# Performance work log

Measured on AMD Instinct MI355X. Metric: run time of the kernel, lower is better.

Reference implementation:

```python
import jax, jax.numpy as jnp
import numpy as np

SQ2PI = 0.79788456
M, D_IN, H1, H2, D_OUT = 256, 784, 256, 256, 10


def setup_inputs() -> dict:
    key = jax.random.key(0)
    ks = jax.random.split(key, 6)
    x = jax.random.normal(ks[0], (M, D_IN), dtype=jnp.float32)
    target = jax.random.randint(ks[1], (M,), 0, D_OUT)

    def init_w(k, fan_in, fan_out):
        # torch init: uniform(-1/sqrt(size(1)), 1/sqrt(size(1))) * scale (scale=1)
        stdv = 1.0 / np.sqrt(fan_out)
        return jax.random.uniform(k, (fan_in, fan_out), jnp.float32, -stdv, stdv)

    w0 = init_w(ks[2], D_IN, H1)
    w1 = init_w(ks[3], H1, H2)
    w2 = init_w(ks[4], H2, H2)
    wlast = init_w(ks[5], H2, D_OUT)
    th0 = jnp.zeros((1, H1), jnp.float32)
    th1 = jnp.zeros((1, H2), jnp.float32)
    th2 = jnp.zeros((1, H2), jnp.float32)
    thlast = jnp.zeros((1, D_OUT), jnp.float32)
    return dict(x=x, target=target, w0=w0, w1=w1, w2=w2, wlast=wlast,
                th0=th0, th1=th1, th2=th2, thlast=thlast)


def _mvg_layer(xbar, xcov, m, th):
    # sigma[b] = m^T @ xcov[b] @ m + diag(sum_j 1 - m[j,:]^2)
    s = jnp.sum(1.0 - m ** 2, axis=0)                      # [H2]
    t = jnp.einsum('bjk,kl->bjl', xcov, m)                 # [B,H,H2]
    sigma = jnp.einsum('ji,bjl->bil', m, t) + jnp.diag(s)[None]  # [B,H2,H2]
    diagsig = jnp.diagonal(sigma, axis1=1, axis2=2)        # [B,H2]
    hbar = xbar @ m + th                                   # [B,H2]
    xbar_next = jnp.tanh(SQ2PI * hbar / jnp.sqrt(diagsig))
    c = (1.0 - xbar_next ** 2) / jnp.sqrt(diagsig)         # [B,H2]
    eye = jnp.eye(m.shape[1], dtype=xbar.dtype)
    xcov_next = (SQ2PI * sigma * c[:, :, None] * c[:, None, :]
                 + eye[None] * (1.0 - xbar_next[:, None, :] ** 2))
    return xbar_next, xcov_next


def reference(x, target, w0, w1, w2, wlast, th0, th1, th2, thlast):
    m0 = 2.0 * jax.nn.sigmoid(w0) - 1.0
    m1 = 2.0 * jax.nn.sigmoid(w1) - 1.0
    m2 = 2.0 * jax.nn.sigmoid(w2) - 1.0
    mlast = 2.0 * jax.nn.sigmoid(wlast) - 1.0

    # first layer: xcov for input is implicitly zero, sigma is diagonal
    diagsig1 = jnp.sum(1.0 - m0 ** 2, axis=0)              # [H1]
    h1bar = x @ m0 + th0                                   # [M,H1]
    x1bar = jnp.tanh(SQ2PI * h1bar / jnp.sqrt(diagsig1))
    eye1 = jnp.eye(m0.shape[1], dtype=x.dtype)
    xcov1 = eye1[None] * (1.0 - x1bar[:, None, :] ** 2)    # [M,H1,H1]

    x2bar, xcov2 = _mvg_layer(x1bar, xcov1, m1, th1)
    x3bar, xcov3 = _mvg_layer(x2bar, xcov2, m2, th2)

    hlastbar = x3bar @ mlast + thlast                      # [M,10]
    logprobs = jax.nn.log_softmax(hlastbar, axis=-1)
    loss = -jnp.mean(jnp.take_along_axis(logprobs, target[:, None], axis=1))
    pred = jnp.argmax(hlastbar, axis=1)
    frac_correct = jnp.mean((pred == target).astype(jnp.float32))
    return (hlastbar, logprobs, xcov3, loss, frac_correct)
```

## Files before the change

kernel.cpp:

```cpp
#include <hip/hip_runtime.h>
#include <hip/hip_fp8.h>
#include <math.h>

#define SQ2PI_F 0.79788456f

typedef __attribute__((ext_vector_type(8))) short short8;
typedef __attribute__((ext_vector_type(4))) float f32x4;
typedef __attribute__((ext_vector_type(4))) unsigned short u16x4;
typedef __attribute__((address_space(1))) unsigned int gas_u32;
typedef __attribute__((address_space(3))) unsigned int las_u32;

__device__ inline unsigned short bf16rne(float x) {
  unsigned int u = __float_as_uint(x);
  u += 0x7fffu + ((u >> 16) & 1u);
  return (unsigned short)(u >> 16);
}
__device__ inline float bf2f(unsigned short u) {
  return __uint_as_float(((unsigned int)u) << 16);
}
__device__ inline unsigned int pk_fp8x4(f32x4 v) {
  __hip_fp8_e4m3 a(v[0]), b(v[1]), c(v[2]), d(v[3]);
  return (unsigned int)a.__x | ((unsigned int)b.__x << 8) |
         ((unsigned int)c.__x << 16) | ((unsigned int)d.__x << 24);
}
__device__ inline float fp8tof(unsigned char b) {
  __hip_fp8_e4m3 h;
  h.__x = (__hip_fp8_storage_t)b;
  return (float)h;
}

__global__ void k_prep(const float* __restrict__ w0, const float* __restrict__ w1,
                       const float* __restrict__ w2, const float* __restrict__ wlast,
                       float* __restrict__ m0, float* __restrict__ m1,
                       unsigned short* __restrict__ m1th, float* __restrict__ m2,
                       unsigned short* __restrict__ m2th, unsigned char* __restrict__ m2f8,
                       float* __restrict__ mlast, float* __restrict__ lf) {
  int b = blockIdx.x, t = threadIdx.x;
  if (b < 784) {
    int i = b * 256 + t;
    m0[i] = tanhf(0.5f * w0[i]);
  } else if (b < 1040) {
    int j = b - 784;
    float v = tanhf(0.5f * w1[j * 256 + t]);
    m1[j * 256 + t] = v;
    m1th[t * 256 + j] = bf16rne(v);
  } else if (b < 1296) {
    int j = b - 1040;
    float v = tanhf(0.5f * w2[j * 256 + t]);
    m2[j * 256 + t] = v;
    m2th[t * 256 + j] = bf16rne(v);
    m2f8[t * 256 + j] = __hip_fp8_e4m3(v).__x;
  } else {
    int i = (b - 1296) * 256 + t;
    if (i < 2560) mlast[i] = tanhf(0.5f * wlast[i]);
    if (b == 1296 && t < 2) lf[t] = 0.f;
  }
}

__global__ void k_layer1(const float* __restrict__ x, const float* __restrict__ m0,
                         const float* __restrict__ th0,
                         float* __restrict__ x1bar, float* __restrict__ d1) {
  __shared__ float xr[784];
  __shared__ float ph[256], pd[256];
  int r = blockIdx.x, t = threadIdx.x;
  int j = t & 255, h = t >> 8;
  for (int p = t; p < 784; p += 512) xr[p] = x[r * 784 + p];
  __syncthreads();
  float acch = 0.f, accd = 0.f;
  int k0 = h * 392, k1 = k0 + 392;
#pragma unroll 8
  for (int k = k0; k < k1; ++k) {
    float mm = m0[k * 256 + j];
    acch = fmaf(xr[k], mm, acch);
    accd = fmaf(-mm, mm, accd + 1.f);
  }
  if (h) { ph[j] = acch; pd[j] = accd; }
  __syncthreads();
  if (!h) {
    acch += ph[j];
    accd += pd[j];
    float rs = rsqrtf(accd);
    float xb = tanhf(SQ2PI_F * (acch + th0[j]) * rs);
    x1bar[r * 256 + j] = xb;
    d1[r * 256 + j] = 1.f - xb * xb;
  }
}

__global__ void k_layer2(const float* __restrict__ d1, const float* __restrict__ x1bar,
                         const float* __restrict__ m1, const float* __restrict__ m2,
                         const float* __restrict__ th1, const float* __restrict__ th2,
                         float* __restrict__ c2, float* __restrict__ d2p,
                         float* __restrict__ h3bar,
                         float* __restrict__ s1g, float* __restrict__ s2g) {
  __shared__ float pd[256], ph[256], ps[256], sx[256], p3[256], q2[256];
  int r = blockIdx.x, t = threadIdx.x;
  int i = t & 255, h = t >> 8;
  int j0 = h * 128, j1 = j0 + 128;
  float accd = 0.f, acch = 0.f, accs = 0.f;
  for (int j = j0; j < j1; ++j) {
    float mm = m1[j * 256 + i];
    accd = fmaf(d1[r * 256 + j] * mm, mm, accd);
    acch = fmaf(x1bar[r * 256 + j], mm, acch);
    accs = fmaf(-mm, mm, accs + 1.f);
  }
  if (h) { pd[i] = accd; ph[i] = acch; ps[i] = accs; }
  __syncthreads();
  if (!h) {
    accd += pd[i];
    acch += ph[i];
    accs += ps[i];
    float rs = rsqrtf(accd + accs);
    float xb = tanhf(SQ2PI_F * (acch + th1[i]) * rs);
    float d = 1.f - xb * xb;
    c2[r * 256 + i] = d * rs;
    d2p[r * 256 + i] = d;
    sx[i] = xb;
    if (r == 0) s1g[i] = accs;
  }
  __syncthreads();
  float acc3 = 0.f, acc2 = 0.f;
  for (int j = j0; j < j1; ++j) {
    float mm = m2[j * 256 + i];
    acc3 = fmaf(sx[j], mm, acc3);
    acc2 = fmaf(-mm, mm, acc2 + 1.f);
  }
  if (h) { p3[i] = acc3; q2[i] = acc2; }
  __syncthreads();
  if (!h) {
    h3bar[r * 256 + i] = acc3 + p3[i] + th2[i];
    if (r == 0) s2g[i] = acc2 + q2[i];
  }
}

__global__ __launch_bounds__(1024) void k_fused(
    const unsigned short* __restrict__ m1th, const unsigned short* __restrict__ m2th,
    const unsigned char* __restrict__ m2f8, const float* __restrict__ d1,
    const float* __restrict__ c2, const float* __restrict__ d2p,
    const float* __restrict__ s1, const float* __restrict__ s2,
    const float* __restrict__ h3bar, float* __restrict__ x3bar,
    float* __restrict__ xcov3) {
  __shared__ __align__(16) unsigned char XC[65536];
  __shared__ __align__(16) unsigned short SB[2][8192];
  __shared__ float c2L[256], d2pL[256], s1L[256], s2L[256];
  __shared__ float c3L[256], d3L[256];
  __shared__ float pq[1024];

  const int b = blockIdx.x;
  const int tid = threadIdx.x;
  const int l = tid & 63, w = tid >> 6;
  const int lr = l & 15, lk = l >> 4;
  const int R = w * 16;

  auto stage_panel = [&](const unsigned short* gsrc, unsigned short* sb) {
    int rl = w * 2 + (l >> 5);
    int ch = l & 31;
    const unsigned short* src = gsrc + rl * 256 + ((ch ^ (rl & 7)) << 3);
    unsigned short* dst = sb + (w * 2) * 256;
    __builtin_amdgcn_global_load_lds((const gas_u32*)src, (las_u32*)dst, 16, 0, 0);
  };

#define PREAD(SBASE, p, kc)                                   \
  (*(const short8*)((const char*)(SBASE) + ((p) << 9) +      \
                    ((unsigned)((((kc) ^ ((p) & 7))) << 4))))

  stage_panel(m1th, SB[0]);

  if (tid < 256) {
    c2L[tid] = c2[b * 256 + tid];
    d2pL[tid] = d2p[b * 256 + tid];
    s1L[tid] = s1[tid];
    s2L[tid] = s2[tid];
  }

  const float* d1b = d1 + b * 256;

  short8 af_w[8];
#pragma unroll
  for (int ks = 0; ks < 8; ++ks) {
    f32x4 dv0 = *(const f32x4*)(d1b + ks * 32 + lk * 8);
    f32x4 dv1 = *(const f32x4*)(d1b + ks * 32 + lk * 8 + 4);
    short8 mv = *(const short8*)(m1th + (size_t)(R + lr) * 256 + ks * 32 + lk * 8);
#pragma unroll
    for (int e = 0; e < 4; ++e) {
      af_w[ks][e] = (short)bf16rne(bf2f((unsigned short)mv[e]) * dv0[e]);
      af_w[ks][e + 4] = (short)bf16rne(bf2f((unsigned short)mv[e + 4]) * dv1[e]);
    }
  }
  __syncthreads();

  short8 afX[8];
  unsigned short(*XB)[8192] = (unsigned short(*)[8192])XC;

#pragma unroll
  for (int cp = 0; cp < 8; ++cp) {
    if (cp < 7)
      stage_panel(m1th + (size_t)(cp + 1) * 8192, SB[(cp + 1) & 1]);
    else
      stage_panel(m2th, SB[0]);
    const unsigned short* sbc = SB[cp & 1];
    f32x4 acc[2];
    acc[0] = {0.f, 0.f, 0.f, 0.f};
    acc[1] = {0.f, 0.f, 0.f, 0.f};
#pragma unroll
    for (int ks = 0; ks < 8; ++ks) {
      short8 bq0 = PREAD(sbc, lr, ks * 4 + lk);
      short8 bq1 = PREAD(sbc, 16 + lr, ks * 4 + lk);
      acc[0] = __builtin_amdgcn_mfma_f32_16x16x32_bf16(af_w[ks], bq0, acc[0], 0, 0, 0);
      acc[1] = __builtin_amdgcn_mfma_f32_16x16x32_bf16(af_w[ks], bq1, acc[1], 0, 0, 0);
    }
    char* XP = (char*)XB[cp & 1];
    int r0 = R + lk * 4;
#pragma unroll
    for (int j = 0; j < 2; ++j) {
      int p = j * 16 + lr;
      int cc = cp * 32 + p;
      float c2c = c2L[cc];
      u16x4 st;
#pragma unroll
      for (int e = 0; e < 4; ++e) {
        int r = r0 + e;
        float g = acc[j][e];
        if (r == cc) g += s1L[r];
        float v = SQ2PI_F * c2L[r] * c2c * g;
        if (r == cc) v += d2pL[r];
        st[e] = bf16rne(v);
      }
      *(u16x4*)(XP + (p << 9) + (((unsigned)(r0 << 1)) ^ ((p & 7) << 4))) = st;
    }
    __syncthreads();
    if (cp == (w >> 1)) {
      int p2 = (w & 1) * 16 + lr;
#pragma unroll
      for (int ks = 0; ks < 8; ++ks) afX[ks] = PREAD(XP, p2, ks * 4 + lk);
    }
  }

#pragma unroll
  for (int lp = 0; lp < 8; ++lp) {
    if (lp < 7) stage_panel(m2th + (size_t)(lp + 1) * 8192, SB[(lp + 1) & 1]);
    const unsigned short* sbt = SB[lp & 1];
    f32x4 at[2];
    at[0] = {0.f, 0.f, 0.f, 0.f};
    at[1] = {0.f, 0.f, 0.f, 0.f};
#pragma unroll
    for (int ks = 0; ks < 8; ++ks) {
      short8 bq0 = PREAD(sbt, lr, ks * 4 + lk);
      short8 bq1 = PREAD(sbt, 16 + lr, ks * 4 + lk);
      at[0] = __builtin_amdgcn_mfma_f32_16x16x32_bf16(afX[ks], bq0, at[0], 0, 0, 0);
      at[1] = __builtin_amdgcn_mfma_f32_16x16x32_bf16(afX[ks], bq1, at[1], 0, 0, 0);
    }
    int j0 = R + lk * 4;
#pragma unroll
    for (int jf = 0; jf < 2; ++jf) {
      int lq = lp * 32 + jf * 16 + lr;
      unsigned int pk = pk_fp8x4(at[jf]);
      *(unsigned int*)(XC + (lq << 8) + ((((j0 >> 3) ^ (lq & 7)) << 3) + (j0 & 7))) = pk;
    }
    __syncthreads();
  }

  {
    int lq = tid >> 2, q = tid & 3;
    float s = 0.f;
#pragma unroll
    for (int jc = q * 8; jc < q * 8 + 8; ++jc) {
      unsigned long long c8 =
          *(const unsigned long long*)(XC + (lq << 8) + ((jc ^ (lq & 7)) << 3));
      short8 mv = *(const short8*)(m2th + (size_t)lq * 256 + jc * 8);
#pragma unroll
      for (int e = 0; e < 8; ++e)
        s = fmaf(bf2f((unsigned short)mv[e]), fp8tof((unsigned char)(c8 >> (8 * e))), s);
    }
    pq[tid] = s;
  }
  __syncthreads();

  if (tid < 256) {
    float ds = pq[tid * 4] + pq[tid * 4 + 1] + pq[tid * 4 + 2] + pq[tid * 4 + 3] + s2L[tid];
    float rs = rsqrtf(ds);
    float xb = tanhf(SQ2PI_F * h3bar[b * 256 + tid] * rs);
    x3bar[b * 256 + tid] = xb;
    float d = 1.f - xb * xb;
    c3L[tid] = d * rs;
    d3L[tid] = d;
  }
  __syncthreads();

  long am2[8];
#pragma unroll
  for (int ks = 0; ks < 8; ++ks)
    am2[ks] = *(const long*)(m2f8 + (size_t)(R + lr) * 256 + ks * 32 + lk * 8);

#pragma unroll
  for (int lp = 0; lp < 8; ++lp) {
    f32x4 sc[2];
    sc[0] = {0.f, 0.f, 0.f, 0.f};
    sc[1] = {0.f, 0.f, 0.f, 0.f};
    int p0 = lp * 32 + lr, p1 = lp * 32 + 16 + lr;
#pragma unroll
    for (int ks = 0; ks < 8; ++ks) {
      long bq0 = *(const long*)(XC + (p0 << 8) + (((ks * 4 + lk) ^ (p0 & 7)) << 3));
      long bq1 = *(const long*)(XC + (p1 << 8) + (((ks * 4 + lk) ^ (p1 & 7)) << 3));
      sc[0] = __builtin_amdgcn_mfma_f32_16x16x32_fp8_fp8(am2[ks], bq0, sc[0], 0, 0, 0);
      sc[1] = __builtin_amdgcn_mfma_f32_16x16x32_fp8_fp8(am2[ks], bq1, sc[1], 0, 0, 0);
    }
    int i0 = R + lk * 4;
#pragma unroll
    for (int lf = 0; lf < 2; ++lf) {
      int gl = lp * 32 + lf * 16 + lr;
      float cg = c3L[gl];
      f32x4 st;
#pragma unroll
      for (int e = 0; e < 4; ++e) {
        int i = i0 + e;
        float g = sc[lf][e];
        if (i == gl) g += s2L[i];
        float v = SQ2PI_F * c3L[i] * cg * g;
        if (i == gl) v += d3L[i];
        st[e] = v;
      }
      *(f32x4*)(xcov3 + ((size_t)b << 16) + (size_t)gl * 256 + i0) = st;
    }
  }
#undef PREAD
}

__global__ void k_final4(const float* __restrict__ x3bar, const float* __restrict__ mlast,
                         const float* __restrict__ thlast, const int* __restrict__ target,
                         float* __restrict__ hlast_out, float* __restrict__ logp_out,
                         float* __restrict__ loss_out, float* __restrict__ frac_out) {
  __shared__ float Wl[2560];
  int t = threadIdx.x;
  int r = blockIdx.x * 64 + t;
  for (int p = t; p < 2560; p += 64) Wl[p] = mlast[p];
  __syncthreads();
  float acc[10];
#pragma unroll
  for (int c = 0; c < 10; ++c) acc[c] = thlast[c];
  for (int j = 0; j < 256; ++j) {
    float xv = x3bar[r * 256 + j];
#pragma unroll
    for (int c = 0; c < 10; ++c) acc[c] = fmaf(xv, Wl[j * 10 + c], acc[c]);
  }
#pragma unroll
  for (int c = 0; c < 10; ++c) hlast_out[r * 10 + c] = acc[c];
  float mx = acc[0];
  int am = 0;
#pragma unroll
  for (int c = 1; c < 10; ++c)
    if (acc[c] > mx) { mx = acc[c]; am = c; }
  float se = 0.f;
#pragma unroll
  for (int c = 0; c < 10; ++c) se += expf(acc[c] - mx);
  float lse = logf(se);
#pragma unroll
  for (int c = 0; c < 10; ++c) logp_out[r * 10 + c] = acc[c] - mx - lse;
  int tg = target[r];
  float lossc = -(acc[tg] - mx - lse) * (1.f / 256.f);
  float corr = (am == tg) ? (1.f / 256.f) : 0.f;
#pragma unroll
  for (int off = 32; off > 0; off >>= 1) {
    lossc += __shfl_down(lossc, off);
    corr += __shfl_down(corr, off);
  }
  if (t == 0) {
    atomicAdd(loss_out, lossc);
    atomicAdd(frac_out, corr);
  }
}


extern "C" void kernel_launch(void* const* d_in, const int* in_sizes, int n_in,
                              void* d_out, int out_size, void* d_ws, size_t ws_size,
                              hipStream_t stream) {
  const float* x = (const float*)d_in[0];
  const int* target = (const int*)d_in[1];
  const float* w0 = (const float*)d_in[2];
  const float* w1 = (const float*)d_in[3];
  const float* w2 = (const float*)d_in[4];
  const float* wlast = (const float*)d_in[5];
  const float* th0 = (const float*)d_in[6];
  const float* th1 = (const float*)d_in[7];
  const float* th2 = (const float*)d_in[8];
  const float* thlast = (const float*)d_in[9];

  float* W = (float*)d_ws;
  size_t o = 0;
  auto alloc = [&](size_t n) { float* p = W + o; o += n; return p; };
  float* m0 = alloc(200704);
  float* m1 = alloc(65536);
  float* m2 = alloc(65536);
  float* mlast = alloc(2560);
  float* s1 = alloc(256);
  float* s2 = alloc(256);
  float* x1bar = alloc(65536);
  float* d1 = alloc(65536);
  float* c2 = alloc(65536);
  float* d2p = alloc(65536);
  float* h3bar = alloc(65536);
  float* x3bar = alloc(65536);
  unsigned short* m1th = (unsigned short*)alloc(32768);
  unsigned short* m2th = (unsigned short*)alloc(32768);
  unsigned char* m2f8 = (unsigned char*)alloc(16384);

  float* hlast = (float*)d_out;
  float* logp = hlast + 2560;
  float* xcov3_out = logp + 2560;
  float* loss = xcov3_out + 16777216;
  float* frac = loss + 1;

  k_prep<<<1306, 256, 0, stream>>>(w0, w1, w2, wlast, m0, m1, m1th, m2, m2th,
                                   m2f8, mlast, loss);
  k_layer1<<<256, 512, 0, stream>>>(x, m0, th0, x1bar, d1);
  k_layer2<<<256, 512, 0, stream>>>(d1, x1bar, m1, m2, th1, th2, c2, d2p,
                                    h3bar, s1, s2);
  k_fused<<<256, 1024, 0, stream>>>(m1th, m2th, m2f8, d1, c2, d2p, s1, s2,
                                    h3bar, x3bar, xcov3_out);
  k_final4<<<4, 64, 0, stream>>>(x3bar, mlast, thlast, target, hlast, logp, loss, frac);
}
```

Measured before the change: 138.8 us.

## Widen panels to 64 columns, fuse diagonal-sigma reduction, pad fp8 tile layout

Doubles the staged weight panel width from 32 to 64 rows, so each wave issues four MFMAs per k-step and the kernel takes half as many panel iterations and barriers. The separate pass that computed the diagonal of sigma from the fp8 tile and global m2 is removed. That sum is now built inside the second GEMM loop from fp32 accumulators and the LDS-staged m2 panel, using shuffles and LDS atomics. The fp8 tile moves from an XOR swizzle to a 264-byte padded row stride, and __launch_bounds__ gains a second argument of 4. LDS use roughly doubles for the staging buffers, and the atomics and wider accumulators raise register and LDS pressure.

```diff
diff --git a/kernel.cpp b/kernel.cpp
--- a/kernel.cpp
+++ b/kernel.cpp
@@ -22,11 +22,6 @@
   __hip_fp8_e4m3 a(v[0]), b(v[1]), c(v[2]), d(v[3]);
   return (unsigned int)a.__x | ((unsigned int)b.__x << 8) |
          ((unsigned int)c.__x << 16) | ((unsigned int)d.__x << 24);
-}
-__device__ inline float fp8tof(unsigned char b) {
-  __hip_fp8_e4m3 h;
-  h.__x = (__hip_fp8_storage_t)b;
-  return (float)h;
 }
 
 __global__ void k_prep(const float* __restrict__ w0, const float* __restrict__ w1,
@@ -132,18 +127,17 @@
   }
 }
 
-__global__ __launch_bounds__(1024) void k_fused(
+__global__ __launch_bounds__(1024, 4) void k_fused(
     const unsigned short* __restrict__ m1th, const unsigned short* __restrict__ m2th,
     const unsigned char* __restrict__ m2f8, const float* __restrict__ d1,
     const float* __restrict__ c2, const float* __restrict__ d2p,
     const float* __restrict__ s1, const float* __restrict__ s2,
     const float* __restrict__ h3bar, float* __restrict__ x3bar,
     float* __restrict__ xcov3) {
-  __shared__ __align__(16) unsigned char XC[65536];
-  __shared__ __align__(16) unsigned short SB[2][8192];
+  __shared__ __align__(16) unsigned char XC[67584];
+  __shared__ __align__(16) unsigned short SB[2][16384];
   __shared__ float c2L[256], d2pL[256], s1L[256], s2L[256];
-  __shared__ float c3L[256], d3L[256];
-  __shared__ float pq[1024];
+  __shared__ float dsig[256], c3L[256], d3L[256];
 
   const int b = blockIdx.x;
   const int tid = threadIdx.x;
@@ -152,11 +146,14 @@
   const int R = w * 16;
 
   auto stage_panel = [&](const unsigned short* gsrc, unsigned short* sb) {
-    int rl = w * 2 + (l >> 5);
-    int ch = l & 31;
-    const unsigned short* src = gsrc + rl * 256 + ((ch ^ (rl & 7)) << 3);
-    unsigned short* dst = sb + (w * 2) * 256;
-    __builtin_amdgcn_global_load_lds((const gas_u32*)src, (las_u32*)dst, 16, 0, 0);
+#pragma unroll
+    for (int q = 0; q < 2; ++q) {
+      int rl = q * 32 + w * 2 + (l >> 5);
+      int ch = l & 31;
+      const unsigned short* src = gsrc + rl * 256 + ((ch ^ (rl & 7)) << 3);
+      unsigned short* dst = sb + (q * 32 + w * 2) * 256;
+      __builtin_amdgcn_global_load_lds((const gas_u32*)src, (las_u32*)dst, 16, 0, 0);
+    }
   };
 
 #define PREAD(SBASE, p, kc)                                   \
@@ -170,6 +167,7 @@
     d2pL[tid] = d2p[b * 256 + tid];
     s1L[tid] = s1[tid];
     s2L[tid] = s2[tid];
+    dsig[tid] = 0.f;
   }
 
   const float* d1b = d1 + b * 256;
@@ -189,31 +187,32 @@
   __syncthreads();
 
   short8 afX[8];
-  unsigned short(*XB)[8192] = (unsigned short(*)[8192])XC;
-
-#pragma unroll
-  for (int cp = 0; cp < 8; ++cp) {
-    if (cp < 7)
-      stage_panel(m1th + (size_t)(cp + 1) * 8192, SB[(cp + 1) & 1]);
+  unsigned short(*XB)[16384] = (unsigned short(*)[16384])XC;
+
+#pragma unroll
+  for (int cp = 0; cp < 4; ++cp) {
+    if (cp < 3)
+      stage_panel(m1th + (size_t)(cp + 1) * 16384, SB[(cp + 1) & 1]);
     else
       stage_panel(m2th, SB[0]);
     const unsigned short* sbc = SB[cp & 1];
-    f32x4 acc[2];
-    acc[0] = {0.f, 0.f, 0.f, 0.f};
-    acc[1] = {0.f, 0.f, 0.f, 0.f};
+    f32x4 acc[4];
+#pragma unroll
+    for (int j = 0; j < 4; ++j) acc[j] = {0.f, 0.f, 0.f, 0.f};
 #pragma unroll
     for (int ks = 0; ks < 8; ++ks) {
-      short8 bq0 = PREAD(sbc, lr, ks * 4 + lk);
-      short8 bq1 = PREAD(sbc, 16 + lr, ks * 4 + lk);
-      acc[0] = __builtin_amdgcn_mfma_f32_16x16x32_bf16(af_w[ks], bq0, acc[0], 0, 0, 0);
-      acc[1] = __builtin_amdgcn_mfma_f32_16x16x32_bf16(af_w[ks], bq1, acc[1], 0, 0, 0);
+#pragma unroll
+      for (int j = 0; j < 4; ++j) {
+        short8 bq = PREAD(sbc, j * 16 + lr, ks * 4 + lk);
+        acc[j] = __builtin_amdgcn_mfma_f32_16x16x32_bf16(af_w[ks], bq, acc[j], 0, 0, 0);
+      }
     }
     char* XP = (char*)XB[cp & 1];
     int r0 = R + lk * 4;
 #pragma unroll
-    for (int j = 0; j < 2; ++j) {
+    for (int j = 0; j < 4; ++j) {
       int p = j * 16 + lr;
-      int cc = cp * 32 + p;
+      int cc = cp * 64 + p;
       float c2c = c2L[cc];
       u16x4 st;
 #pragma unroll
@@ -228,55 +227,49 @@
       *(u16x4*)(XP + (p << 9) + (((unsigned)(r0 << 1)) ^ ((p & 7) << 4))) = st;
     }
     __syncthreads();
-    if (cp == (w >> 1)) {
-      int p2 = (w & 1) * 16 + lr;
+    if (cp == (w >> 2)) {
+      int p2 = (w & 3) * 16 + lr;
 #pragma unroll
       for (int ks = 0; ks < 8; ++ks) afX[ks] = PREAD(XP, p2, ks * 4 + lk);
     }
   }
 
 #pragma unroll
-  for (int lp = 0; lp < 8; ++lp) {
-    if (lp < 7) stage_panel(m2th + (size_t)(lp + 1) * 8192, SB[(lp + 1) & 1]);
+  for (int lp = 0; lp < 4; ++lp) {
+    if (lp < 3) stage_panel(m2th + (size_t)(lp + 1) * 16384, SB[(lp + 1) & 1]);
     const unsigned short* sbt = SB[lp & 1];
-    f32x4 at[2];
-    at[0] = {0.f, 0.f, 0.f, 0.f};
-    at[1] = {0.f, 0.f, 0.f, 0.f};
+    f32x4 at[4];
+#pragma unroll
+    for (int j = 0; j < 4; ++j) at[j] = {0.f, 0.f, 0.f, 0.f};
 #pragma unroll
     for (int ks = 0; ks < 8; ++ks) {
-      short8 bq0 = PREAD(sbt, lr, ks * 4 + lk);
-      short8 bq1 = PREAD(sbt, 16 + lr, ks * 4 + lk);
-      at[0] = __builtin_amdgcn_mfma_f32_16x16x32_bf16(afX[ks], bq0, at[0], 0, 0, 0);
-      at[1] = __builtin_amdgcn_mfma_f32_16x16x32_bf16(afX[ks], bq1, at[1], 0, 0, 0);
+#pragma unroll
+      for (int j = 0; j < 4; ++j) {
+        short8 bq = PREAD(sbt, j * 16 + lr, ks * 4 + lk);
+        at[j] = __builtin_amdgcn_mfma_f32_16x16x32_bf16(afX[ks], bq, at[j], 0, 0, 0);
+      }
     }
     int j0 = R + lk * 4;
 #pragma unroll
-    for (int jf = 0; jf < 2; ++jf) {
-      int lq = lp * 32 + jf * 16 + lr;
-      unsigned int pk = pk_fp8x4(at[jf]);
-      *(unsigned int*)(XC + (lq << 8) + ((((j0 >> 3) ^ (lq & 7)) << 3) + (j0 & 7))) = pk;
+    for (int jf = 0; jf < 4; ++jf) {
+      int p = jf * 16 + lr;
+      int lq = lp * 64 + p;
+      *(unsigned int*)(XC + (size_t)lq * 264 + j0) = pk_fp8x4(at[jf]);
+      const char* mb = (const char*)sbt + (p << 9) +
+                       ((((j0 >> 3) ^ (p & 7))) << 4) + ((j0 & 7) << 1);
+      u16x4 mv = *(const u16x4*)mb;
+      float s = 0.f;
+#pragma unroll
+      for (int e = 0; e < 4; ++e) s = fmaf(bf2f(mv[e]), at[jf][e], s);
+      s += __shfl_xor(s, 16, 64);
+      s += __shfl_xor(s, 32, 64);
+      if (lk == 0) atomicAdd(&dsig[lq], s);
     }
     __syncthreads();
   }
 
-  {
-    int lq = tid >> 2, q = tid & 3;
-    float s = 0.f;
-#pragma unroll
-    for (int jc = q * 8; jc < q * 8 + 8; ++jc) {
-      unsigned long long c8 =
-          *(const unsigned long long*)(XC + (lq << 8) + ((jc ^ (lq & 7)) << 3));
-      short8 mv = *(const short8*)(m2th + (size_t)lq * 256 + jc * 8);
-#pragma unroll
-      for (int e = 0; e < 8; ++e)
-        s = fmaf(bf2f((unsigned short)mv[e]), fp8tof((unsigned char)(c8 >> (8 * e))), s);
-    }
-    pq[tid] = s;
-  }
-  __syncthreads();
-
   if (tid < 256) {
-    float ds = pq[tid * 4] + pq[tid * 4 + 1] + pq[tid * 4 + 2] + pq[tid * 4 + 3] + s2L[tid];
+    float ds = dsig[tid] + s2L[tid];
     float rs = rsqrtf(ds);
     float xb = tanhf(SQ2PI_F * h3bar[b * 256 + tid] * rs);
     x3bar[b * 256 + tid] = xb;
@@ -292,22 +285,23 @@
     am2[ks] = *(const long*)(m2f8 + (size_t)(R + lr) * 256 + ks * 32 + lk * 8);
 
 #pragma unroll
-  for (int lp = 0; lp < 8; ++lp) {
-    f32x4 sc[2];
-    sc[0] = {0.f, 0.f, 0.f, 0.f};
-    sc[1] = {0.f, 0.f, 0.f, 0.f};
-    int p0 = lp * 32 + lr, p1 = lp * 32 + 16 + lr;
+  for (int lp = 0; lp < 4; ++lp) {
+    f32x4 sc[4];
+#pragma unroll
+    for (int j = 0; j < 4; ++j) sc[j] = {0.f, 0.f, 0.f, 0.f};
 #pragma unroll
     for (int ks = 0; ks < 8; ++ks) {
-      long bq0 = *(const long*)(XC + (p0 << 8) + (((ks * 4 + lk) ^ (p0 & 7)) << 3));
-      long bq1 = *(const long*)(XC + (p1 << 8) + (((ks * 4 + lk) ^ (p1 & 7)) << 3));
-      sc[0] = __builtin_amdgcn_mfma_f32_16x16x32_fp8_fp8(am2[ks], bq0, sc[0], 0, 0, 0);
-      sc[1] = __builtin_amdgcn_mfma_f32_16x16x32_fp8_fp8(am2[ks], bq1, sc[1], 0, 0, 0);
+#pragma unroll
+      for (int j = 0; j < 4; ++j) {
+        int p = lp * 64 + j * 16 + lr;
+        long bq = *(const long*)(XC + (size_t)p * 264 + (ks * 4 + lk) * 8);
+        sc[j] = __builtin_amdgcn_mfma_f32_16x16x32_fp8_fp8(am2[ks], bq, sc[j], 0, 0, 0);
+      }
     }
     int i0 = R + lk * 4;
 #pragma unroll
-    for (int lf = 0; lf < 2; ++lf) {
-      int gl = lp * 32 + lf * 16 + lr;
+    for (int lf = 0; lf < 4; ++lf) {
+      int gl = lp * 64 + lf * 16 + lr;
       float cg = c3L[gl];
       f32x4 st;
 #pragma unroll
```

Result: no change. 138.3 us (-0.4%).
